# Kernel optimization log

Hardware: AMD Instinct MI355X
Metric: run time of the kernel (lower is better)

## Reference

```python
import jax, jax.numpy as jnp
import numpy as np

D_MODEL = 1024
N_HEADS = 16
D_FF = 4096
LN_EPS = 1e-5


def _linear_params(key, d_in, d_out):
    kw, kb = jax.random.split(key)
    bound = 1.0 / np.sqrt(d_in)
    W = jax.random.uniform(kw, (d_out, d_in), jnp.float32, -bound, bound)
    b = jax.random.uniform(kb, (d_out,), jnp.float32, -bound, bound)
    return W, b


def setup_inputs() -> dict:
    key = jax.random.key(0)
    ks = jax.random.split(key, 8)
    x = jax.random.normal(ks[0], (2, 2048, D_MODEL), jnp.float32)
    Wq, bq = _linear_params(ks[1], D_MODEL, D_MODEL)
    Wk, bk = _linear_params(ks[2], D_MODEL, D_MODEL)
    Wv, bv = _linear_params(ks[3], D_MODEL, D_MODEL)
    Wo, bo = _linear_params(ks[4], D_MODEL, D_MODEL)
    W1, b1 = _linear_params(ks[5], D_MODEL, D_FF)
    W2, b2 = _linear_params(ks[6], D_FF, D_MODEL)
    ln1_g = jnp.ones((D_MODEL,), jnp.float32)
    ln1_b = jnp.zeros((D_MODEL,), jnp.float32)
    ln2_g = jnp.ones((D_MODEL,), jnp.float32)
    ln2_b = jnp.zeros((D_MODEL,), jnp.float32)
    return dict(x=x, Wq=Wq, bq=bq, Wk=Wk, bk=bk, Wv=Wv, bv=bv, Wo=Wo, bo=bo,
                ln1_g=ln1_g, ln1_b=ln1_b, W1=W1, b1=b1, W2=W2, b2=b2,
                ln2_g=ln2_g, ln2_b=ln2_b)


def _layernorm(x, g, b):
    mu = jnp.mean(x, axis=-1, keepdims=True)
    var = jnp.mean(jnp.square(x - mu), axis=-1, keepdims=True)
    return (x - mu) * jax.lax.rsqrt(var + LN_EPS) * g + b


def _lin(x, W, b):
    return jnp.einsum('bsd,ed->bse', x, W) + b


def _attn(x, Wq, bq, Wk, bk, Wv, bv, Wo, bo):
    B, S, _ = x.shape
    d_head = D_MODEL // N_HEADS
    scale = d_head ** -0.5
    split = lambda t: t.reshape(B, S, N_HEADS, d_head).transpose(0, 2, 1, 3)
    q = split(_lin(x, Wq, bq))  # b h s d
    k = split(_lin(x, Wk, bk))
    v = split(_lin(x, Wv, bv))
    scores = jnp.einsum('bhqd,bhkd->bhqk', q, k) * scale
    attn = jax.nn.softmax(scores, axis=-1)
    out = jnp.einsum('bhqk,bhkd->bhqd', attn, v)
    out = out.transpose(0, 2, 1, 3).reshape(B, S, D_MODEL)
    return _lin(out, Wo, bo)


def reference(x, Wq, bq, Wk, bk, Wv, bv, Wo, bo, ln1_g, ln1_b, W1, b1, W2, b2, ln2_g, ln2_b):
    x = x + _attn(_layernorm(x, ln1_g, ln1_b), Wq, bq, Wk, bk, Wv, bv, Wo, bo)
    h = _layernorm(x, ln2_g, ln2_b)
    h = _lin(h, W1, b1)
    h = jax.nn.gelu(h, approximate=False)
    h = _lin(h, W2, b2)
    return x + h
```

## Files before the change

kernel.cpp:

```cpp
#include <hip/hip_runtime.h>
#include <hip/hip_bf16.h>
#include <stdint.h>

#define DM 1024
#define DFF 4096
#define NH 16
#define DH 64
#define SEQ 2048
#define MROWS 4096

typedef unsigned short u16;
typedef __attribute__((ext_vector_type(8))) short bf16x8;
typedef __attribute__((ext_vector_type(4))) float f32x4;
typedef __attribute__((ext_vector_type(16))) float f32x16;
typedef __attribute__((ext_vector_type(4))) unsigned short u16x4;

__device__ __forceinline__ u16 f2b(float f) {
  union { float f; uint32_t u; } v; v.f = f;
  uint32_t r = v.u + 0x7FFFu + ((v.u >> 16) & 1u);
  return (u16)(r >> 16);
}

__device__ __forceinline__ u16 f2bn(float f) {
  __hip_bfloat16 h = __float2bfloat16(f);
  return *reinterpret_cast<u16*>(&h);
}

__device__ __forceinline__ uint32_t pk2(float lo, float hi) {
  return (uint32_t)f2bn(lo) | ((uint32_t)f2bn(hi) << 16);
}

__device__ __forceinline__ void gl_lds16(const void* g, void* l) {
  __builtin_amdgcn_global_load_lds(
      (const __attribute__((address_space(1))) uint32_t*)g,
      (__attribute__((address_space(3))) uint32_t*)l, 16, 0, 0);
}

struct CvtArgs { const float* src[6]; u16* dst[6]; int n4[6]; };

__global__ void cvt_kernel(CvtArgs a) {
  const int stride = gridDim.x * blockDim.x;
  const int t0 = blockIdx.x * blockDim.x + threadIdx.x;
  for (int i = 0; i < 6; ++i) {
    const float4* s = (const float4*)a.src[i];
    u16x4* d = (u16x4*)a.dst[i];
    const int n = a.n4[i];
    for (int idx = t0; idx < n; idx += stride) {
      float4 v = s[idx];
      u16x4 o;
      o[0] = f2b(v.x); o[1] = f2b(v.y); o[2] = f2b(v.z); o[3] = f2b(v.w);
      d[idx] = o;
    }
  }
}

__global__ __launch_bounds__(256)
void ln_kernel(const float* __restrict__ x, const float* __restrict__ g,
               const float* __restrict__ be, u16* __restrict__ out) {
  const int row = blockIdx.x;
  const int tid = threadIdx.x;
  const float4 v = ((const float4*)(x + (size_t)row * DM))[tid];
  float s  = v.x + v.y + v.z + v.w;
  float s2 = v.x * v.x + v.y * v.y + v.z * v.z + v.w * v.w;
  #pragma unroll
  for (int m = 1; m < 64; m <<= 1) {
    s  += __shfl_xor(s,  m, 64);
    s2 += __shfl_xor(s2, m, 64);
  }
  __shared__ float red[8];
  const int w = tid >> 6, lane = tid & 63;
  if (lane == 0) { red[w] = s; red[4 + w] = s2; }
  __syncthreads();
  s  = red[0] + red[1] + red[2] + red[3];
  s2 = red[4] + red[5] + red[6] + red[7];
  const float mu  = s * (1.0f / DM);
  const float var = s2 * (1.0f / DM) - mu * mu;
  const float rstd = rsqrtf(var + 1e-5f);
  const float4 gv = ((const float4*)g)[tid];
  const float4 bv = ((const float4*)be)[tid];
  u16x4 o;
  o[0] = f2b((v.x - mu) * rstd * gv.x + bv.x);
  o[1] = f2b((v.y - mu) * rstd * gv.y + bv.y);
  o[2] = f2b((v.z - mu) * rstd * gv.z + bv.z);
  o[3] = f2b((v.w - mu) * rstd * gv.w + bv.w);
  ((u16x4*)(out + (size_t)row * DM))[tid] = o;
}

__global__ __launch_bounds__(256)
void combine_kernel(const float4* __restrict__ p0, const float4* __restrict__ p1,
                    const float4* __restrict__ bias, const float4* __restrict__ resid,
                    float4* __restrict__ out, int total4, int colmask4) {
  for (int i = blockIdx.x * 256 + threadIdx.x; i < total4; i += gridDim.x * 256) {
    float4 a = p0[i], b = p1[i], bs = bias[i & colmask4], rr = resid[i];
    float4 o;
    o.x = a.x + b.x + bs.x + rr.x;
    o.y = a.y + b.y + bs.y + rr.y;
    o.z = a.z + b.z + bs.z + rr.z;
    o.w = a.w + b.w + bs.w + rr.w;
    out[i] = o;
  }
}

__global__ __launch_bounds__(256)
void combine_ln_kernel(const float4* __restrict__ p0, const float4* __restrict__ p1,
                       const float4* __restrict__ bias, const float4* __restrict__ resid,
                       float4* __restrict__ xout,
                       const float* __restrict__ g, const float* __restrict__ be,
                       u16* __restrict__ nout) {
  const int row = blockIdx.x;
  const int tid = threadIdx.x;
  const int i = row * (DM / 4) + tid;
  const float4 a = p0[i], b = p1[i], bs = bias[tid], rr = resid[i];
  float4 v;
  v.x = a.x + b.x + bs.x + rr.x;
  v.y = a.y + b.y + bs.y + rr.y;
  v.z = a.z + b.z + bs.z + rr.z;
  v.w = a.w + b.w + bs.w + rr.w;
  xout[i] = v;
  float s  = v.x + v.y + v.z + v.w;
  float s2 = v.x * v.x + v.y * v.y + v.z * v.z + v.w * v.w;
  #pragma unroll
  for (int m = 1; m < 64; m <<= 1) {
    s  += __shfl_xor(s,  m, 64);
    s2 += __shfl_xor(s2, m, 64);
  }
  __shared__ float red[8];
  const int w = tid >> 6, lane = tid & 63;
  if (lane == 0) { red[w] = s; red[4 + w] = s2; }
  __syncthreads();
  s  = red[0] + red[1] + red[2] + red[3];
  s2 = red[4] + red[5] + red[6] + red[7];
  const float mu  = s * (1.0f / DM);
  const float var = s2 * (1.0f / DM) - mu * mu;
  const float rstd = rsqrtf(var + 1e-5f);
  const float4 gv = ((const float4*)g)[tid];
  const float4 bv = ((const float4*)be)[tid];
  u16x4 o;
  o[0] = f2b((v.x - mu) * rstd * gv.x + bv.x);
  o[1] = f2b((v.y - mu) * rstd * gv.y + bv.y);
  o[2] = f2b((v.z - mu) * rstd * gv.z + bv.z);
  o[3] = f2b((v.w - mu) * rstd * gv.w + bv.w);
  ((u16x4*)(nout + (size_t)row * DM))[tid] = o;
}

struct GemmPtrs { const u16* W[3]; const float* bias[3]; void* out[3];
                  const float* resid; int vtrans; };

template<int EPI>
__global__ __launch_bounds__(256)
void gemm_bt(const u16* __restrict__ A, GemmPtrs p, int M, int N,
             int Kstride, int Kchunk) {
  __shared__ __align__(16) u16 As[128 * 64];
  __shared__ __align__(16) u16 Bs[128 * 64];
  const u16* __restrict__ Wm = p.W[blockIdx.z];
  const float* __restrict__ bias = p.bias[blockIdx.z];
  void* outv = p.out[blockIdx.z];
  const float* resid = p.resid;

  const int tid = threadIdx.x;
  const int lane = tid & 63;
  const int w = tid >> 6;
  const int brow = blockIdx.y * 128;
  const int bcol = blockIdx.x * 128;
  const int wr = (w >> 1) * 64, wc = (w & 1) * 64;
  const int koff = (EPI == 3) ? blockIdx.z * Kchunk : 0;

  f32x4 acc[4][4] = {};

  const int srow = lane >> 3;
  const int scol = (lane & 7) * 8;
  const int nkt = Kchunk >> 6;
  for (int kt = 0; kt < nkt; ++kt) {
    const int k0 = koff + kt * 64;
    #pragma unroll
    for (int i = 0; i < 4; ++i) {
      const int r = i * 32 + w * 8;
      gl_lds16(&A [(size_t)(brow + r + srow) * Kstride + k0 + scol], &As[r * 64]);
      gl_lds16(&Wm[(size_t)(bcol + r + srow) * Kstride + k0 + scol], &Bs[r * 64]);
    }
    __syncthreads();
    #pragma unroll
    for (int ks = 0; ks < 2; ++ks) {
      const int ko = ks * 32 + (lane >> 4) * 8;
      bf16x8 a[4], b[4];
      #pragma unroll
      for (int f = 0; f < 4; ++f)
        a[f] = *(const bf16x8*)&As[(wr + f * 16 + (lane & 15)) * 64 + ko];
      #pragma unroll
      for (int f = 0; f < 4; ++f)
        b[f] = *(const bf16x8*)&Bs[(wc + f * 16 + (lane & 15)) * 64 + ko];
      #pragma unroll
      for (int fr = 0; fr < 4; ++fr)
        #pragma unroll
        for (int fc = 0; fc < 4; ++fc)
          acc[fr][fc] = __builtin_amdgcn_mfma_f32_16x16x32_bf16(a[fr], b[fc], acc[fr][fc], 0, 0, 0);
    }
    __syncthreads();
  }

  const int orow0 = brow + wr + (lane >> 4) * 4;
  const int ocol0 = bcol + wc + (lane & 15);

  if (EPI == 0 && p.vtrans && blockIdx.z == 2) {
    #pragma unroll
    for (int fr = 0; fr < 4; ++fr) {
      const int row0 = orow0 + fr * 16;
      const int bq = row0 >> 11, s0 = row0 & (SEQ - 1);
      #pragma unroll
      for (int fc = 0; fc < 4; ++fc) {
        const int col = ocol0 + fc * 16;
        const float bvv = bias[col];
        u16x4 o;
        #pragma unroll
        for (int r = 0; r < 4; ++r) o[r] = f2b(acc[fr][fc][r] + bvv);
        *(u16x4*)((u16*)outv + (size_t)(bq * DM + col) * SEQ + s0) = o;
      }
    }
    return;
  }

  const float oscale = (EPI == 0 && p.vtrans && blockIdx.z == 0) ? 0.125f : 1.0f;

  #pragma unroll
  for (int fr = 0; fr < 4; ++fr) {
    #pragma unroll
    for (int fc = 0; fc < 4; ++fc) {
      const int col = ocol0 + fc * 16;
      const float bvv = (EPI == 3) ? 0.0f : bias[col];
      #pragma unroll
      for (int r = 0; r < 4; ++r) {
        const int row = orow0 + fr * 16 + r;
        const size_t idx = (size_t)row * N + col;
        float v = acc[fr][fc][r] + bvv;
        if (EPI == 0) {
          ((u16*)outv)[idx] = f2b(v * oscale);
        } else if (EPI == 1) {
          float ge = 0.5f * v * (1.0f + erff(v * 0.70710678118654752f));
          ((u16*)outv)[idx] = f2b(ge);
        } else if (EPI == 2) {
          ((float*)outv)[idx] = v + resid[idx];
        } else {
          ((float*)outv)[idx] = v;
        }
      }
    }
  }
}

__global__ __launch_bounds__(128, 4)
void attn_kernel(const u16* __restrict__ Q, const u16* __restrict__ K,
                 const u16* __restrict__ Vt, float* __restrict__ Opart,
                 float2* __restrict__ ML) {
  __shared__ __align__(16) u16 Ks[64 * 64];
  __shared__ __align__(16) u16 Vts[64 * 64];
  const int tid = threadIdx.x, lane = tid & 63, w = tid >> 6;
  const int bh = blockIdx.y, b = bh >> 4, h = bh & 15;
  const int kvh = blockIdx.z;
  const int q0 = blockIdx.x * 64 + w * 32;
  const size_t base = (size_t)b * SEQ * DM + (size_t)h * DH;
  const size_t vbase = (size_t)(b * DM + h * DH) * SEQ;
  float* __restrict__ Op = Opart + (size_t)kvh * MROWS * DM;
  float2* __restrict__ mlp = ML + (size_t)kvh * 2 * NH * SEQ;

  const int l31 = lane & 31, hi = lane >> 5, l7 = l31 & 7;

  bf16x8 qf[4];
  {
    const size_t qrow = base + (size_t)(q0 + l31) * DM;
    #pragma unroll
    for (int dt = 0; dt < 4; ++dt)
      qf[dt] = *(const bf16x8*)&Q[qrow + dt * 16 + hi * 8];
  }

  f32x16 oacc[2] = {};
  float mq = -1e30f, lq = 0.0f;

  for (int kt = kvh * (SEQ / 128); kt < (kvh + 1) * (SEQ / 128); ++kt) {
    #pragma unroll
    for (int i = 0; i < 4; ++i) {
      const int r0 = w * 32 + i * 8;
      const int row = r0 + (lane >> 3);
      const int ch = ((lane & 7) ^ (row & 7)) * 8;
      gl_lds16(&K[base + (size_t)(kt * 64 + row) * DM + ch], &Ks[r0 * 64]);
      gl_lds16(&Vt[vbase + (size_t)row * SEQ + kt * 64 + ch], &Vts[r0 * 64]);
    }
    __syncthreads();

    #pragma unroll
    for (int sub = 0; sub < 2; ++sub) {
      f32x16 sacc = {};
      __builtin_amdgcn_s_setprio(1);
      #pragma unroll
      for (int dt = 0; dt < 4; ++dt) {
        bf16x8 kf = *(const bf16x8*)&Ks[(sub * 32 + l31) * 64 + (((dt << 1) | hi) ^ l7) * 8];
        sacc = __builtin_amdgcn_mfma_f32_32x32x16_bf16(kf, qf[dt], sacc, 0, 0, 0);
      }
      __builtin_amdgcn_s_setprio(0);

      float tm = sacc[0];
      #pragma unroll
      for (int r = 1; r < 16; ++r) tm = fmaxf(tm, sacc[r]);
      tm = fmaxf(tm, __shfl_xor(tm, 32, 64));

      if (__any(tm > mq + 8.0f)) {
        const float mnew = fmaxf(mq, tm);
        const float fs = __expf(mq - mnew);
        mq = mnew;
        lq *= fs;
        #pragma unroll
        for (int r = 0; r < 16; ++r) {
          const float fsr = __shfl(fs, (r & 3) + 8 * (r >> 2) + 4 * hi, 64);
          oacc[0][r] *= fsr;
          oacc[1][r] *= fsr;
        }
      }

      uint32_t wd[2][4];
      float ps = 0.0f;
      #pragma unroll
      for (int half = 0; half < 2; ++half) {
        float p[8];
        #pragma unroll
        for (int j = 0; j < 8; ++j) {
          p[j] = __expf(sacc[half * 8 + j] - mq);
          ps += p[j];
        }
        const uint32_t a = pk2(p[0], p[1]), c = pk2(p[2], p[3]);
        const uint32_t bb = pk2(p[4], p[5]), d = pk2(p[6], p[7]);
        const uint32_t xa = (uint32_t)__shfl_xor((int)a, 32, 64);
        const uint32_t xb = (uint32_t)__shfl_xor((int)bb, 32, 64);
        const uint32_t xc = (uint32_t)__shfl_xor((int)c, 32, 64);
        const uint32_t xd = (uint32_t)__shfl_xor((int)d, 32, 64);
        wd[half][0] = hi ? xb : a;
        wd[half][1] = hi ? xd : c;
        wd[half][2] = hi ? bb : xa;
        wd[half][3] = hi ? d : xc;
      }
      lq += ps;
      bf16x8 pa0, pa1;
      #pragma unroll
      for (int j = 0; j < 4; ++j) {
        ((uint32_t*)&pa0)[j] = wd[0][j];
        ((uint32_t*)&pa1)[j] = wd[1][j];
      }

      __builtin_amdgcn_s_setprio(1);
      #pragma unroll
      for (int dt = 0; dt < 2; ++dt) {
        #pragma unroll
        for (int ks = 0; ks < 2; ++ks) {
          bf16x8 vf = *(const bf16x8*)&Vts[(dt * 32 + l31) * 64 +
                                           (((sub << 2) | (ks << 1) | hi) ^ l7) * 8];
          oacc[dt] = __builtin_amdgcn_mfma_f32_32x32x16_bf16(ks ? pa1 : pa0, vf, oacc[dt], 0, 0, 0);
        }
      }
      __builtin_amdgcn_s_setprio(0);
    }
    __syncthreads();
  }

  const float ltot = lq + __shfl_xor(lq, 32, 64);
  #pragma unroll
  for (int r = 0; r < 16; ++r) {
    const int crow = (r & 3) + 8 * (r >> 2) + 4 * hi;
    const size_t orow = base + (size_t)(q0 + crow) * DM;
    Op[orow + l31]      = oacc[0][r];
    Op[orow + 32 + l31] = oacc[1][r];
  }
  if (hi == 0) mlp[(size_t)bh * SEQ + q0 + l31] = make_float2(mq, ltot);
}

__global__ __launch_bounds__(256)
void attn_merge(const float4* __restrict__ Op0, const float4* __restrict__ Op1,
                const float2* __restrict__ ML, u16* __restrict__ ao) {
  const int row = blockIdx.x, tid = threadIdx.x;
  const int idx4 = row * (DM / 4) + tid;
  const int bh = ((row >> 11) << 4) | (tid >> 4);
  const int s = row & (SEQ - 1);
  const float2 a = ML[(size_t)bh * SEQ + s];
  const float2 c = ML[(size_t)(2 * NH) * SEQ + (size_t)bh * SEQ + s];
  const float m = fmaxf(a.x, c.x);
  const float f0 = __expf(a.x - m), f1 = __expf(c.x - m);
  const float inv = 1.0f / (a.y * f0 + c.y * f1);
  const float4 o0 = Op0[idx4], o1 = Op1[idx4];
  u16x4 o;
  o[0] = f2bn((o0.x * f0 + o1.x * f1) * inv);
  o[1] = f2bn((o0.y * f0 + o1.y * f1) * inv);
  o[2] = f2bn((o0.z * f0 + o1.z * f1) * inv);
  o[3] = f2bn((o0.w * f0 + o1.w * f1) * inv);
  ((u16x4*)ao)[idx4] = o;
}

extern "C" void kernel_launch(void* const* d_in, const int* in_sizes, int n_in,
                              void* d_out, int out_size, void* d_ws, size_t ws_size,
                              hipStream_t stream) {
  const float* x    = (const float*)d_in[0];
  const float* Wq   = (const float*)d_in[1];
  const float* bq   = (const float*)d_in[2];
  const float* Wk   = (const float*)d_in[3];
  const float* bk   = (const float*)d_in[4];
  const float* Wv   = (const float*)d_in[5];
  const float* bv   = (const float*)d_in[6];
  const float* Wo   = (const float*)d_in[7];
  const float* bo   = (const float*)d_in[8];
  const float* ln1g = (const float*)d_in[9];
  const float* ln1b = (const float*)d_in[10];
  const float* W1   = (const float*)d_in[11];
  const float* b1   = (const float*)d_in[12];
  const float* W2   = (const float*)d_in[13];
  const float* b2   = (const float*)d_in[14];
  const float* ln2g = (const float*)d_in[15];
  const float* ln2b = (const float*)d_in[16];
  float* out = (float*)d_out;

  char* wsb = (char*)d_ws;
  size_t off = 0;
  auto alloc = [&](size_t bytes) -> char* {
    char* pp = wsb + off;
    off += (bytes + 255) & ~(size_t)255;
    return pp;
  };
  u16* Wq_b = (u16*)alloc((size_t)DM * DM * 2);
  u16* Wk_b = (u16*)alloc((size_t)DM * DM * 2);
  u16* Wv_b = (u16*)alloc((size_t)DM * DM * 2);
  u16* Wo_b = (u16*)alloc((size_t)DM * DM * 2);
  u16* W1_b = (u16*)alloc((size_t)DFF * DM * 2);
  u16* W2_b = (u16*)alloc((size_t)DM * DFF * 2);
  u16* xn   = (u16*)alloc((size_t)MROWS * DM * 2);
  u16* qb   = (u16*)alloc((size_t)MROWS * DM * 2);
  u16* kb   = (u16*)alloc((size_t)MROWS * DM * 2);
  u16* vt   = (u16*)alloc((size_t)MROWS * DM * 2);
  u16* ao   = (u16*)alloc((size_t)MROWS * DM * 2);
  u16* h1   = (u16*)alloc((size_t)MROWS * DFF * 2);
  float2* ml = (float2*)alloc((size_t)2 * 2 * NH * SEQ * sizeof(float2));

  float* pA = (float*)xn;
  float* pB = (float*)kb;
  float* attnOp = (float*)h1;

  CvtArgs ca;
  ca.src[0] = Wq; ca.dst[0] = Wq_b; ca.n4[0] = DM * DM / 4;
  ca.src[1] = Wk; ca.dst[1] = Wk_b; ca.n4[1] = DM * DM / 4;
  ca.src[2] = Wv; ca.dst[2] = Wv_b; ca.n4[2] = DM * DM / 4;
  ca.src[3] = Wo; ca.dst[3] = Wo_b; ca.n4[3] = DM * DM / 4;
  ca.src[4] = W1; ca.dst[4] = W1_b; ca.n4[4] = DFF * DM / 4;
  ca.src[5] = W2; ca.dst[5] = W2_b; ca.n4[5] = DM * DFF / 4;
  cvt_kernel<<<2048, 256, 0, stream>>>(ca);

  ln_kernel<<<MROWS, 256, 0, stream>>>(x, ln1g, ln1b, xn);

  GemmPtrs pq = {};
  pq.W[0] = Wq_b; pq.W[1] = Wk_b; pq.W[2] = Wv_b;
  pq.bias[0] = bq; pq.bias[1] = bk; pq.bias[2] = bv;
  pq.out[0] = qb; pq.out[1] = kb; pq.out[2] = vt;
  pq.vtrans = 1;
  gemm_bt<0><<<dim3(DM / 128, MROWS / 128, 3), 256, 0, stream>>>(xn, pq, MROWS, DM, DM, DM);

  attn_kernel<<<dim3(SEQ / 64, 2 * NH, 2), 128, 0, stream>>>(qb, kb, vt, attnOp, ml);
  attn_merge<<<MROWS, 256, 0, stream>>>((const float4*)attnOp,
                                        (const float4*)(attnOp + (size_t)MROWS * DM),
                                        (const float2*)ml, ao);

  GemmPtrs po = {};
  po.W[0] = Wo_b; po.W[1] = Wo_b;
  po.bias[0] = bo; po.bias[1] = bo;
  po.out[0] = pA; po.out[1] = pB;
  gemm_bt<3><<<dim3(DM / 128, MROWS / 128, 2), 256, 0, stream>>>(ao, po, MROWS, DM, DM, DM / 2);
  combine_ln_kernel<<<MROWS, 256, 0, stream>>>((const float4*)pA, (const float4*)pB,
                                               (const float4*)bo, (const float4*)x,
                                               (float4*)out, ln2g, ln2b, ao);

  GemmPtrs p1 = {};
  p1.W[0] = W1_b; p1.bias[0] = b1; p1.out[0] = h1;
  gemm_bt<1><<<dim3(DFF / 128, MROWS / 128, 1), 256, 0, stream>>>(ao, p1, MROWS, DFF, DM, DM);

  GemmPtrs p2 = {};
  p2.W[0] = W2_b; p2.W[1] = W2_b;
  p2.bias[0] = b2; p2.bias[1] = b2;
  p2.out[0] = pA; p2.out[1] = pB;
  gemm_bt<3><<<dim3(DM / 128, MROWS / 128, 2), 256, 0, stream>>>(h1, p2, MROWS, DM, DFF, DFF / 2);
  combine_kernel<<<2048, 256, 0, stream>>>((const float4*)pA, (const float4*)pB,
                                           (const float4*)b2, (const float4*)out,
                                           (float4*)out, MROWS * DM / 4, DM / 4 - 1);
}
```

Before: 304.5 us.

## Triple-buffer GEMM LDS tiles with async prefetch and XOR-swizzled layout

Replaces the single-buffered K=64 tile loop in the shared GEMM kernel with a three-stage ring of K=32 tiles. Loads for tile t+2 are issued while tile t is computed, and explicit vmcnt waits plus one barrier per step replace the two syncthreads. The LDS layout is XOR-swizzled to cut bank conflicts on fragment reads. This hides global-load latency behind MFMA work, at the cost of more LDS use, twice as many loop iterations, and reliance on hand-written waitcnt counts.

After: 301.5 us. No clear change (-1.0%).

```diff
diff --git a/kernel.cpp b/kernel.cpp
--- a/kernel.cpp
+++ b/kernel.cpp
@@ -150,8 +150,8 @@
 __global__ __launch_bounds__(256)
 void gemm_bt(const u16* __restrict__ A, GemmPtrs p, int M, int N,
              int Kstride, int Kchunk) {
-  __shared__ __align__(16) u16 As[128 * 64];
-  __shared__ __align__(16) u16 Bs[128 * 64];
+  __shared__ __align__(16) u16 As[3][128 * 32];
+  __shared__ __align__(16) u16 Bs[3][128 * 32];
   const u16* __restrict__ Wm = p.W[blockIdx.z];
   const float* __restrict__ bias = p.bias[blockIdx.z];
   void* outv = p.out[blockIdx.z];
@@ -167,35 +167,45 @@
 
   f32x4 acc[4][4] = {};
 
-  const int srow = lane >> 3;
-  const int scol = (lane & 7) * 8;
-  const int nkt = Kchunk >> 6;
-  for (int kt = 0; kt < nkt; ++kt) {
-    const int k0 = koff + kt * 64;
-    #pragma unroll
-    for (int i = 0; i < 4; ++i) {
-      const int r = i * 32 + w * 8;
-      gl_lds16(&A [(size_t)(brow + r + srow) * Kstride + k0 + scol], &As[r * 64]);
-      gl_lds16(&Wm[(size_t)(bcol + r + srow) * Kstride + k0 + scol], &Bs[r * 64]);
-    }
-    __syncthreads();
-    #pragma unroll
-    for (int ks = 0; ks < 2; ++ks) {
-      const int ko = ks * 32 + (lane >> 4) * 8;
-      bf16x8 a[4], b[4];
-      #pragma unroll
-      for (int f = 0; f < 4; ++f)
-        a[f] = *(const bf16x8*)&As[(wr + f * 16 + (lane & 15)) * 64 + ko];
-      #pragma unroll
-      for (int f = 0; f < 4; ++f)
-        b[f] = *(const bf16x8*)&Bs[(wc + f * 16 + (lane & 15)) * 64 + ko];
-      #pragma unroll
-      for (int fr = 0; fr < 4; ++fr)
-        #pragma unroll
-        for (int fc = 0; fc < 4; ++fc)
-          acc[fr][fc] = __builtin_amdgcn_mfma_f32_16x16x32_bf16(a[fr], b[fc], acc[fr][fc], 0, 0, 0);
-    }
-    __syncthreads();
+  const int srow = tid >> 2;
+  const int sc = (((tid & 3) ^ ((tid >> 3) & 3))) * 8;
+  const int ldso = w * 512;
+
+  const int nt = Kchunk >> 5;
+
+  auto stage = [&](int t) {
+    const int rs = t % 3;
+    const int k0 = koff + t * 32;
+    gl_lds16(&A [(size_t)(brow + srow) * Kstride + k0 + sc],      &As[rs][ldso]);
+    gl_lds16(&A [(size_t)(brow + 64 + srow) * Kstride + k0 + sc], &As[rs][2048 + ldso]);
+    gl_lds16(&Wm[(size_t)(bcol + srow) * Kstride + k0 + sc],      &Bs[rs][ldso]);
+    gl_lds16(&Wm[(size_t)(bcol + 64 + srow) * Kstride + k0 + sc], &Bs[rs][2048 + ldso]);
+  };
+
+  stage(0);
+  if (nt > 1) stage(1);
+
+  for (int t = 0; t < nt; ++t) {
+    if (t + 1 < nt) asm volatile("s_waitcnt vmcnt(4) lgkmcnt(0)" ::: "memory");
+    else            asm volatile("s_waitcnt vmcnt(0) lgkmcnt(0)" ::: "memory");
+    __builtin_amdgcn_s_barrier();
+    __builtin_amdgcn_sched_barrier(0);
+    if (t + 2 < nt) stage(t + 2);
+
+    const int rs = t % 3;
+    bf16x8 a[4], b[4];
+    #pragma unroll
+    for (int f = 0; f < 4; ++f) {
+      const int ra = wr + f * 16 + (lane & 15);
+      a[f] = *(const bf16x8*)&As[rs][ra * 32 + ((lane >> 4) ^ ((ra >> 1) & 3)) * 8];
+      const int rb = wc + f * 16 + (lane & 15);
+      b[f] = *(const bf16x8*)&Bs[rs][rb * 32 + ((lane >> 4) ^ ((rb >> 1) & 3)) * 8];
+    }
+    #pragma unroll
+    for (int fr = 0; fr < 4; ++fr)
+      #pragma unroll
+      for (int fc = 0; fc < 4; ++fc)
+        acc[fr][fc] = __builtin_amdgcn_mfma_f32_16x16x32_bf16(a[fr], b[fc], acc[fr][fc], 0, 0, 0);
   }
 
   const int orow0 = brow + wr + (lane >> 4) * 4;
```
